# Kernel optimization log

Measured on AMD Instinct MI355X. Metric: run time of the kernel, lower is better.

The kernel has to match this reference:

```python
import jax, jax.numpy as jnp
import numpy as np

TEMPERATURE = 0.07
BASE_TEMPERATURE = 0.07


def _pairwise_euclid(x):
    # torch.cdist(x, x, p=2), with safe sqrt (zero grad at zero distance)
    sq = jnp.sum(x * x, axis=1)
    d2 = sq[:, None] + sq[None, :] - 2.0 * (x @ x.T)
    d2 = jnp.maximum(d2, 0.0)
    safe = jnp.where(d2 > 0.0, d2, 1.0)
    return jnp.where(d2 > 0.0, jnp.sqrt(safe), 0.0)


def setup_inputs() -> dict:
    key = jax.random.key(0)
    k1, k2 = jax.random.split(key)
    features = jax.random.normal(k1, (1024, 2, 512), dtype=jnp.float32)
    labels = jax.random.uniform(k2, (1024,), dtype=jnp.float32)
    return {"features": features, "labels": labels}


def reference(features, labels):
    B, V, D = features.shape
    N = B * V
    # torch.cat(torch.unbind(features, dim=1), dim=0): views stacked -> [N, D]
    cf = features.transpose(1, 0, 2).reshape(N, D)
    lab = jnp.tile(labels, V)  # label of row i is labels[i % B]

    dist = _pairwise_euclid(cf)              # [N, N]
    logits = -dist / TEMPERATURE
    eye = jnp.eye(N, dtype=logits.dtype)
    w = jnp.exp(logits) * (1.0 - eye)        # exp(logits) with l == i excluded

    dis = jnp.abs(lab[:, None] - lab[None, :])  # |y_i - y_j|, symmetric

    # negative[i, j] = sum_{l != i, |y_l - y_i| >= |y_i - y_j|} exp(logits[i, l])
    # computed per-row via sort + suffix cumsum + searchsorted (O(N^2 log N))
    order = jnp.argsort(dis, axis=1)
    sorted_d = jnp.take_along_axis(dis, order, axis=1)
    sorted_w = jnp.take_along_axis(w, order, axis=1)
    suffix = jnp.flip(jnp.cumsum(jnp.flip(sorted_w, axis=1), axis=1), axis=1)
    suffix = jnp.concatenate([suffix, jnp.zeros((N, 1), suffix.dtype)], axis=1)  # [N, N+1]
    # side='left': counts entries strictly < d, so suffix[idx] sums all >= d (ties incl.)
    idx = jax.vmap(lambda sd, d: jnp.searchsorted(sd, d, side='left'))(sorted_d, dis)
    negative = jnp.take_along_axis(suffix, idx, axis=1)
    negative = negative * (1.0 - eye) + eye  # diag set to 1 (log -> 0)

    logits_z = logits * (1.0 - eye)          # logits[i, i] = 0
    log_prob = logits_z - jnp.log(negative)
    mean_log_prob_pos = jnp.sum(log_prob, axis=1) / (N - 1)
    loss = -(TEMPERATURE / BASE_TEMPERATURE) * jnp.mean(mean_log_prob_pos)
    return loss
```

## Files before the change

kernel.cpp:

```cpp
#include <hip/hip_runtime.h>
#include <math.h>


#define NN 2048
#define BB 1024
#define DD 512
#define NT 256
#define NEGINF (-INFINITY)
#define CS 64.0f

typedef short s16x8 __attribute__((ext_vector_type(8)));
typedef float f32x4 __attribute__((ext_vector_type(4)));

__device__ __forceinline__ const float* cf_row(const float* F, int i) {
    return F + ((size_t)(i & (BB - 1)) * 2 + (size_t)(i >> 10)) * DD;
}

__device__ __forceinline__ unsigned bf_rne(float x) {
    const unsigned u = __float_as_uint(x);
    return (u + 0x7FFFu + ((u >> 16) & 1u)) >> 16;
}
__device__ __forceinline__ float bf_val(unsigned h) {
    return __uint_as_float(h << 16);
}

__global__ __launch_bounds__(256) void rank_sort_kernel(const float* __restrict__ labels,
                                                        float* __restrict__ slab,
                                                        int* __restrict__ sj) {
    __shared__ float lab[BB];
    const int t = threadIdx.x;
    #pragma unroll
    for (int e = 0; e < 4; ++e) lab[t + e * NT] = labels[t + e * NT];
    __syncthreads();
    const int p = blockIdx.x * NT + t;
    const float L = lab[p];
    int rank = 0;
    #pragma unroll 4
    for (int q4 = 0; q4 < BB / 4; ++q4) {
        const float4 l4 = reinterpret_cast<const float4*>(lab)[q4];
        const int q = q4 * 4;
        rank += (l4.x < L) || (l4.x == L && (q + 0) < p);
        rank += (l4.y < L) || (l4.y == L && (q + 1) < p);
        rank += (l4.z < L) || (l4.z == L && (q + 2) < p);
        rank += (l4.w < L) || (l4.w == L && (q + 3) < p);
    }
    slab[2 * rank] = L; slab[2 * rank + 1] = L;
    sj[2 * rank] = p;   sj[2 * rank + 1] = p + BB;
}

__global__ __launch_bounds__(256) void prep_split_kernel(const float* __restrict__ F,
                                                         ushort* __restrict__ Ahi,
                                                         ushort* __restrict__ Alo,
                                                         float* __restrict__ sq) {
    const int t = threadIdx.x;
    const int lane = t & 63;
    const int w = t >> 6;
    const int i = blockIdx.x * 4 + w;
    const float* src = cf_row(F, i);
    const float4 v0 = reinterpret_cast<const float4*>(src)[lane];
    const float4 v1 = reinterpret_cast<const float4*>(src)[lane + 64];
    float ss = v0.x * v0.x + v0.y * v0.y + v0.z * v0.z + v0.w * v0.w
             + v1.x * v1.x + v1.y * v1.y + v1.z * v1.z + v1.w * v1.w;
    #pragma unroll
    for (int st = 32; st > 0; st >>= 1) ss += __shfl_down(ss, st);
    if (lane == 0) sq[i] = ss;

    const float a[8] = {v0.x, v0.y, v0.z, v0.w, v1.x, v1.y, v1.z, v1.w};
    ushort h[8], l[8];
    #pragma unroll
    for (int e = 0; e < 8; ++e) {
        const unsigned hb = bf_rne(a[e]);
        h[e] = (ushort)hb;
        l[e] = (ushort)bf_rne(a[e] - bf_val(hb));
    }
    const size_t base = (size_t)i * DD;
    *reinterpret_cast<ushort4*>(&Ahi[base + lane * 4])       = make_ushort4(h[0], h[1], h[2], h[3]);
    *reinterpret_cast<ushort4*>(&Ahi[base + 256 + lane * 4]) = make_ushort4(h[4], h[5], h[6], h[7]);
    *reinterpret_cast<ushort4*>(&Alo[base + lane * 4])       = make_ushort4(l[0], l[1], l[2], l[3]);
    *reinterpret_cast<ushort4*>(&Alo[base + 256 + lane * 4]) = make_ushort4(l[4], l[5], l[6], l[7]);
}

#define GT 64
#define TK 32
__global__ __launch_bounds__(256) void gemm_dist_kernel(const ushort* __restrict__ Ahi,
                                                        const ushort* __restrict__ Alo,
                                                        const float* __restrict__ sq,
                                                        const int* __restrict__ sj,
                                                        float* __restrict__ distp) {
    __shared__ ushort Ah[4][GT][8];
    __shared__ ushort Al[4][GT][8];
    __shared__ ushort Bh[4][GT][8];
    __shared__ ushort Bl[4][GT][8];
    __shared__ int   sjcA[GT];
    __shared__ int   sjcB[GT];
    __shared__ float sqA[GT];
    __shared__ float sqB[GT];

    const int t = threadIdx.x;
    const int lane = t & 63;
    const int w = t >> 6;

    const int id = blockIdx.x;
    int by = (int)((__fsqrt_rn(8.0f * (float)id + 1.0f) - 1.0f) * 0.5f);
    while ((by + 1) * (by + 2) / 2 <= id) ++by;
    while (by * (by + 1) / 2 > id) --by;
    const int bx = id - by * (by + 1) / 2;
    const int row0 = by * GT;
    const int col0 = bx * GT;
    const bool diag = (bx == by);

    if (t < GT) {
        const int s = sj[row0 + t];
        sjcA[t] = s; sqA[t] = sq[s];
    } else if (t < 2 * GT) {
        const int u = t - GT;
        const int s = sj[col0 + u];
        sjcB[u] = s; sqB[u] = sq[s];
    }
    __syncthreads();
    const int rr = t >> 2;
    const int cq = t & 3;
    const size_t gA = (size_t)sjcA[rr] * DD + cq * 8;
    const size_t gB = (size_t)sjcB[rr] * DD + cq * 8;

    f32x4 acc[4] = {};
    const int m = lane & 15;
    const int q = lane >> 4;

    for (int kt = 0; kt < DD / TK; ++kt) {
        __syncthreads();
        const size_t ko = (size_t)kt * TK;
        *reinterpret_cast<int4*>(&Ah[cq][rr][0]) = *reinterpret_cast<const int4*>(&Ahi[gA + ko]);
        *reinterpret_cast<int4*>(&Al[cq][rr][0]) = *reinterpret_cast<const int4*>(&Alo[gA + ko]);
        *reinterpret_cast<int4*>(&Bh[cq][rr][0]) = *reinterpret_cast<const int4*>(&Ahi[gB + ko]);
        *reinterpret_cast<int4*>(&Bl[cq][rr][0]) = *reinterpret_cast<const int4*>(&Alo[gB + ko]);
        __syncthreads();

        const s16x8 fah = *reinterpret_cast<const s16x8*>(&Ah[q][w * 16 + m][0]);
        const s16x8 fal = *reinterpret_cast<const s16x8*>(&Al[q][w * 16 + m][0]);
        s16x8 fbh[4], fbl[4];
        #pragma unroll
        for (int nt = 0; nt < 4; ++nt) {
            fbh[nt] = *reinterpret_cast<const s16x8*>(&Bh[q][nt * 16 + m][0]);
            fbl[nt] = *reinterpret_cast<const s16x8*>(&Bl[q][nt * 16 + m][0]);
        }
        #pragma unroll
        for (int nt = 0; nt < 4; ++nt) {
            acc[nt] = __builtin_amdgcn_mfma_f32_16x16x32_bf16(fah, fbh[nt], acc[nt], 0, 0, 0);
            acc[nt] = __builtin_amdgcn_mfma_f32_16x16x32_bf16(fah, fbl[nt], acc[nt], 0, 0, 0);
            acc[nt] = __builtin_amdgcn_mfma_f32_16x16x32_bf16(fal, fbh[nt], acc[nt], 0, 0, 0);
        }
    }

    const int lr0 = w * 16 + q * 4;
    #pragma unroll
    for (int nt = 0; nt < 4; ++nt) {
        const int lc = nt * 16 + m;
        float o[4];
        #pragma unroll
        for (int r = 0; r < 4; ++r) {
            const float d2 = sqA[lr0 + r] + sqB[lc] - 2.0f * acc[nt][r];
            o[r] = (d2 > 0.f) ? sqrtf(d2) : 0.f;
        }
        #pragma unroll
        for (int r = 0; r < 4; ++r)
            distp[(size_t)(row0 + lr0 + r) * NN + col0 + lc] = o[r];
        if (!diag) {
            const float4 o4 = make_float4(o[0], o[1], o[2], o[3]);
            *reinterpret_cast<float4*>(&distp[(size_t)(col0 + lc) * NN + row0 + lr0]) = o4;
        }
    }
}

__device__ __forceinline__ int bs_right(const float* key, float d, int lo, int hi) {
    while (lo < hi) {
        const int mid = (lo + hi) >> 1;
        if (key[mid] >= d) hi = mid; else lo = mid + 1;
    }
    return lo;
}
__device__ __forceinline__ int bs_left(const float* key, float d, int lo, int hi) {
    while (lo < hi) {
        const int mid = (lo + hi) >> 1;
        if (key[mid] < d) hi = mid; else lo = mid + 1;
    }
    return lo;
}

__global__ __launch_bounds__(256) void row_kernel(const float* __restrict__ distp,
                                                  const float* __restrict__ slab,
                                                  double* __restrict__ rowval) {
    __shared__ float key[NN];
    __shared__ float Pf[NN];
    __shared__ float Sf[NN + 1];
    __shared__ float wmxA[4], wmxB[4], wps[4], wss[4];
    __shared__ double wDA[4], wLA[4], wDB[4], wLB[4];

    const int pr = blockIdx.x;
    const int rA = 2 * pr, rB = 2 * pr + 1;
    const int t = threadIdx.x;
    const int lane = t & 63;
    const int w = t >> 6;
    const float x = slab[rA];
    const float negInvT = -1.0f / 0.07f;
    const float* drowA = &distp[(size_t)rA * NN];
    const float* drowB = &distp[(size_t)rB * NN];

    #pragma unroll
    for (int e = 0; e < 2; ++e) {
        const int p4 = t + e * NT;
        const float4 l4 = reinterpret_cast<const float4*>(slab)[p4];
        key[p4 * 4 + 0] = fabsf(l4.x - x);
        key[p4 * 4 + 1] = fabsf(l4.y - x);
        key[p4 * 4 + 2] = fabsf(l4.z - x);
        key[p4 * 4 + 3] = fabsf(l4.w - x);
    }
    const int cb = t * 8;
    float vA[8], vB[8];
    double dsumA = 0.0, dsumB = 0.0;
    float mxA = NEGINF, mxB = NEGINF;
    #pragma unroll
    for (int e = 0; e < 2; ++e) {
        const float4 a4 = reinterpret_cast<const float4*>(drowA)[2 * t + e];
        const float4 b4 = reinterpret_cast<const float4*>(drowB)[2 * t + e];
        const float av[4] = {a4.x, a4.y, a4.z, a4.w};
        const float bv[4] = {b4.x, b4.y, b4.z, b4.w};
        #pragma unroll
        for (int c = 0; c < 4; ++c) {
            const int pc = cb + e * 4 + c;
            if (pc == rA) vA[e * 4 + c] = NEGINF;
            else { const float vv = av[c] * negInvT; vA[e * 4 + c] = vv; mxA = fmaxf(mxA, vv); dsumA += (double)av[c]; }
            if (pc == rB) vB[e * 4 + c] = NEGINF;
            else { const float vv = bv[c] * negInvT; vB[e * 4 + c] = vv; mxB = fmaxf(mxB, vv); dsumB += (double)bv[c]; }
        }
    }
    #pragma unroll
    for (int st = 32; st > 0; st >>= 1) {
        mxA = fmaxf(mxA, __shfl_down(mxA, st));
        mxB = fmaxf(mxB, __shfl_down(mxB, st));
    }
    if (lane == 0) { wmxA[w] = mxA; wmxB[w] = mxB; }
    __syncthreads();
    const float MA = fmaxf(fmaxf(wmxA[0], wmxA[1]), fmaxf(wmxA[2], wmxA[3]));
    const float MB = fmaxf(fmaxf(wmxB[0], wmxB[1]), fmaxf(wmxB[2], wmxB[3]));

    int L8[8], R8[8];
    const int a = cb, b = cb + 7;
    {
        const int le = (rA - 1 < b) ? rA - 1 : b;
        if (a <= le) {
            const float da = key[a];
            const int Ra = bs_right(key, da, rA, NN);
            int Rl = Ra;
            if (le > a) Rl = bs_right(key, key[le], rA, Ra);
            for (int p = a; p <= le; ++p) {
                const float d = key[p];
                int R;
                if (p == a) R = Ra;
                else if (p == le) R = Rl;
                else R = bs_right(key, d, Rl, Ra);
                int L = p + 1;
                while (L < rA && key[L] == d) ++L;
                L8[p - a] = L; R8[p - a] = R;
            }
        }
        const int rs = (rA + 1 > a) ? rA + 1 : a;
        if (rs <= b) {
            const float dr = key[rs];
            const int Lr = bs_left(key, dr, 0, rA);
            int Lb = Lr;
            if (b > rs) Lb = bs_left(key, key[b], 0, Lr);
            for (int p = rs; p <= b; ++p) {
                const float d = key[p];
                int L;
                if (p == rs) L = Lr;
                else if (p == b) L = Lb;
                else L = bs_left(key, d, Lb, Lr);
                int R = p;
                while (R > rA && key[R - 1] == d) --R;
                L8[p - a] = L; R8[p - a] = R;
            }
        }
        if (rA >= a && rA <= b) { L8[rA - a] = rA; R8[rA - a] = rA; }
    }

    double lnsumA = 0.0;
    {
        float e8[8];
        #pragma unroll
        for (int jj = 0; jj < 8; ++jj) e8[jj] = __expf(vA[jj] - MA + CS);
        {
            float run = 0.f, ex[8];
            #pragma unroll
            for (int jj = 0; jj < 8; ++jj) { ex[jj] = run; run += e8[jj]; }
            float inc = run;
            #pragma unroll
            for (int st = 1; st < 64; st <<= 1) {
                const float nm = __shfl_up(inc, st);
                if (lane >= st) inc += nm;
            }
            float xofs = __shfl_up(inc, 1);
            if (lane == 0) xofs = 0.f;
            if (lane == 63) wps[w] = inc;
            __syncthreads();
            #pragma unroll
            for (int ww = 0; ww < 3; ++ww)
                if (ww < w) xofs += wps[ww];
            #pragma unroll
            for (int jj = 0; jj < 8; ++jj) Pf[cb + jj] = ex[jj] + xofs;
        }
        {
            float run = 0.f, sx[8];
            #pragma unroll
            for (int jj = 7; jj >= 0; --jj) { run += e8[jj]; sx[jj] = run; }
            float inc = run;
            #pragma unroll
            for (int st = 1; st < 64; st <<= 1) {
                const float nm = __shfl_down(inc, st);
                if (lane + st < 64) inc += nm;
            }
            float xofs = __shfl_down(inc, 1);
            if (lane == 63) xofs = 0.f;
            if (lane == 0) wss[w] = inc;
            __syncthreads();
            #pragma unroll
            for (int ww = 1; ww < 4; ++ww)
                if (ww > w) xofs += wss[ww];
            #pragma unroll
            for (int jj = 0; jj < 8; ++jj) Sf[cb + jj] = sx[jj] + xofs;
            if (t == 0) Sf[NN] = 0.f;
        }
        __syncthreads();
        const float MBA = MA - CS;
        #pragma unroll
        for (int jj = 0; jj < 8; ++jj) {
            const int p = cb + jj;
            if (p == rA) continue;
            const float s = fmaxf(Pf[L8[jj]] + Sf[R8[jj]], 1e-38f);
            lnsumA += (double)(MBA + __logf(s));
        }
    }
    __syncthreads();

    double lnsumB = 0.0;
    {
        float e8[8];
        #pragma unroll
        for (int jj = 0; jj < 8; ++jj) e8[jj] = __expf(vB[jj] - MB + CS);
        {
            float run = 0.f, ex[8];
            #pragma unroll
            for (int jj = 0; jj < 8; ++jj) { ex[jj] = run; run += e8[jj]; }
            float inc = run;
            #pragma unroll
            for (int st = 1; st < 64; st <<= 1) {
                const float nm = __shfl_up(inc, st);
                if (lane >= st) inc += nm;
            }
            float xofs = __shfl_up(inc, 1);
            if (lane == 0) xofs = 0.f;
            if (lane == 63) wps[w] = inc;
            __syncthreads();
            #pragma unroll
            for (int ww = 0; ww < 3; ++ww)
                if (ww < w) xofs += wps[ww];
            #pragma unroll
            for (int jj = 0; jj < 8; ++jj) Pf[cb + jj] = ex[jj] + xofs;
        }
        {
            float run = 0.f, sx[8];
            #pragma unroll
            for (int jj = 7; jj >= 0; --jj) { run += e8[jj]; sx[jj] = run; }
            float inc = run;
            #pragma unroll
            for (int st = 1; st < 64; st <<= 1) {
                const float nm = __shfl_down(inc, st);
                if (lane + st < 64) inc += nm;
            }
            float xofs = __shfl_down(inc, 1);
            if (lane == 63) xofs = 0.f;
            if (lane == 0) wss[w] = inc;
            __syncthreads();
            #pragma unroll
            for (int ww = 1; ww < 4; ++ww)
                if (ww > w) xofs += wss[ww];
            #pragma unroll
            for (int jj = 0; jj < 8; ++jj) Sf[cb + jj] = sx[jj] + xofs;
            if (t == 0) Sf[NN] = 0.f;
        }
        __syncthreads();
        const float MBB = MB - CS;
        #pragma unroll
        for (int jj = 0; jj < 8; ++jj) {
            const int p = cb + jj;
            if (p == rB) continue;
            const float s = fmaxf(Pf[L8[jj]] + Sf[R8[jj]], 1e-38f);
            lnsumB += (double)(MBB + __logf(s));
        }
    }

    #pragma unroll
    for (int st = 32; st > 0; st >>= 1) {
        dsumA  += __shfl_down(dsumA, st);
        lnsumA += __shfl_down(lnsumA, st);
        dsumB  += __shfl_down(dsumB, st);
        lnsumB += __shfl_down(lnsumB, st);
    }
    if (lane == 0) { wDA[w] = dsumA; wLA[w] = lnsumA; wDB[w] = dsumB; wLB[w] = lnsumB; }
    __syncthreads();
    if (t == 0) {
        rowval[rA] = (-(wDA[0] + wDA[1] + wDA[2] + wDA[3]) / 0.07)
                   - (wLA[0] + wLA[1] + wLA[2] + wLA[3]);
        rowval[rB] = (-(wDB[0] + wDB[1] + wDB[2] + wDB[3]) / 0.07)
                   - (wLB[0] + wLB[1] + wLB[2] + wLB[3]);
    }
}

__global__ __launch_bounds__(256) void finalize_kernel(const double* __restrict__ rowval,
                                                       float* __restrict__ out) {
    __shared__ double red[NT];
    const int t = threadIdx.x;
    double s = 0.0;
    for (int j = t; j < NN; j += NT) s += rowval[j];
    red[t] = s;
    __syncthreads();
    for (int ofs = NT / 2; ofs > 0; ofs >>= 1) {
        if (t < ofs) red[t] += red[t + ofs];
        __syncthreads();
    }
    if (t == 0) {
        out[0] = (float)(-red[0] / ((double)NN * (double)(NN - 1)));
    }
}

extern "C" void kernel_launch(void* const* d_in, const int* in_sizes, int n_in,
                              void* d_out, int out_size, void* d_ws, size_t ws_size,
                              hipStream_t stream) {
    const float* features = (const float*)d_in[0];
    const float* labels   = (const float*)d_in[1];
    float* out = (float*)d_out;

    char* ws = (char*)d_ws;
    size_t off = 0;
    float*  sq     = (float*) (ws + off); off += NN * sizeof(float);
    float*  slab   = (float*) (ws + off); off += NN * sizeof(float);
    int*    sj     = (int*)   (ws + off); off += NN * sizeof(int);
    double* rowval = (double*)(ws + off); off += NN * sizeof(double);
    ushort* Ahi    = (ushort*)(ws + off); off += (size_t)NN * DD * sizeof(ushort);
    ushort* Alo    = (ushort*)(ws + off); off += (size_t)NN * DD * sizeof(ushort);
    float*  distp  = (float*) (ws + off); off += (size_t)NN * NN * sizeof(float);

    rank_sort_kernel<<<4, NT, 0, stream>>>(labels, slab, sj);
    prep_split_kernel<<<NN / 4, NT, 0, stream>>>(features, Ahi, Alo, sq);
    gemm_dist_kernel<<<32 * 33 / 2, NT, 0, stream>>>(Ahi, Alo, sq, sj, distp);
    row_kernel<<<NN / 2, NT, 0, stream>>>(distp, slab, rowval);
    finalize_kernel<<<1, NT, 0, stream>>>(rowval, out);
}
```

Before: 137.5 us.

## Fuse label-rank and prep kernels; double-buffer GEMM shared tiles

Merges the label ranking kernel and the bf16 hi/lo split kernel into one launch, using block index to select the role, removing a kernel launch. The distance GEMM now double-buffers its shared-memory K tiles with one barrier per iteration, loading the next tile while the MFMAs run on the current one. This doubles shared memory per block and adds register pressure for the in-flight loads.

After: 135.6 us. About the same (-1.4%).

```diff
diff --git a/kernel.cpp b/kernel.cpp
--- a/kernel.cpp
+++ b/kernel.cpp
@@ -6,6 +6,7 @@
 #define BB 1024
 #define DD 512
 #define NT 256
+#define NPREP 512
 #define NEGINF (-INFINITY)
 #define CS 64.0f
 
@@ -24,60 +25,60 @@
     return __uint_as_float(h << 16);
 }
 
-__global__ __launch_bounds__(256) void rank_sort_kernel(const float* __restrict__ labels,
-                                                        float* __restrict__ slab,
-                                                        int* __restrict__ sj) {
-    __shared__ float lab[BB];
+__global__ __launch_bounds__(256) void prep_kernel(const float* __restrict__ F,
+                                                   const float* __restrict__ labels,
+                                                   ushort* __restrict__ Ahi,
+                                                   ushort* __restrict__ Alo,
+                                                   float* __restrict__ sq,
+                                                   float* __restrict__ slab,
+                                                   int* __restrict__ sj) {
     const int t = threadIdx.x;
-    #pragma unroll
-    for (int e = 0; e < 4; ++e) lab[t + e * NT] = labels[t + e * NT];
-    __syncthreads();
-    const int p = blockIdx.x * NT + t;
-    const float L = lab[p];
-    int rank = 0;
-    #pragma unroll 4
-    for (int q4 = 0; q4 < BB / 4; ++q4) {
-        const float4 l4 = reinterpret_cast<const float4*>(lab)[q4];
-        const int q = q4 * 4;
-        rank += (l4.x < L) || (l4.x == L && (q + 0) < p);
-        rank += (l4.y < L) || (l4.y == L && (q + 1) < p);
-        rank += (l4.z < L) || (l4.z == L && (q + 2) < p);
-        rank += (l4.w < L) || (l4.w == L && (q + 3) < p);
-    }
-    slab[2 * rank] = L; slab[2 * rank + 1] = L;
-    sj[2 * rank] = p;   sj[2 * rank + 1] = p + BB;
-}
-
-__global__ __launch_bounds__(256) void prep_split_kernel(const float* __restrict__ F,
-                                                         ushort* __restrict__ Ahi,
-                                                         ushort* __restrict__ Alo,
-                                                         float* __restrict__ sq) {
-    const int t = threadIdx.x;
-    const int lane = t & 63;
-    const int w = t >> 6;
-    const int i = blockIdx.x * 4 + w;
-    const float* src = cf_row(F, i);
-    const float4 v0 = reinterpret_cast<const float4*>(src)[lane];
-    const float4 v1 = reinterpret_cast<const float4*>(src)[lane + 64];
-    float ss = v0.x * v0.x + v0.y * v0.y + v0.z * v0.z + v0.w * v0.w
-             + v1.x * v1.x + v1.y * v1.y + v1.z * v1.z + v1.w * v1.w;
-    #pragma unroll
-    for (int st = 32; st > 0; st >>= 1) ss += __shfl_down(ss, st);
-    if (lane == 0) sq[i] = ss;
-
-    const float a[8] = {v0.x, v0.y, v0.z, v0.w, v1.x, v1.y, v1.z, v1.w};
-    ushort h[8], l[8];
-    #pragma unroll
-    for (int e = 0; e < 8; ++e) {
-        const unsigned hb = bf_rne(a[e]);
-        h[e] = (ushort)hb;
-        l[e] = (ushort)bf_rne(a[e] - bf_val(hb));
-    }
-    const size_t base = (size_t)i * DD;
-    *reinterpret_cast<ushort4*>(&Ahi[base + lane * 4])       = make_ushort4(h[0], h[1], h[2], h[3]);
-    *reinterpret_cast<ushort4*>(&Ahi[base + 256 + lane * 4]) = make_ushort4(h[4], h[5], h[6], h[7]);
-    *reinterpret_cast<ushort4*>(&Alo[base + lane * 4])       = make_ushort4(l[0], l[1], l[2], l[3]);
-    *reinterpret_cast<ushort4*>(&Alo[base + 256 + lane * 4]) = make_ushort4(l[4], l[5], l[6], l[7]);
+    if (blockIdx.x < NPREP) {
+        const int lane = t & 63;
+        const int w = t >> 6;
+        const int i = blockIdx.x * 4 + w;
+        const float* src = cf_row(F, i);
+        const float4 v0 = reinterpret_cast<const float4*>(src)[lane];
+        const float4 v1 = reinterpret_cast<const float4*>(src)[lane + 64];
+        float ss = v0.x * v0.x + v0.y * v0.y + v0.z * v0.z + v0.w * v0.w
+                 + v1.x * v1.x + v1.y * v1.y + v1.z * v1.z + v1.w * v1.w;
+        #pragma unroll
+        for (int st = 32; st > 0; st >>= 1) ss += __shfl_down(ss, st);
+        if (lane == 0) sq[i] = ss;
+
+        const float a[8] = {v0.x, v0.y, v0.z, v0.w, v1.x, v1.y, v1.z, v1.w};
+        ushort h[8], l[8];
+        #pragma unroll
+        for (int e = 0; e < 8; ++e) {
+            const unsigned hb = bf_rne(a[e]);
+            h[e] = (ushort)hb;
+            l[e] = (ushort)bf_rne(a[e] - bf_val(hb));
+        }
+        const size_t base = (size_t)i * DD;
+        *reinterpret_cast<ushort4*>(&Ahi[base + lane * 4])       = make_ushort4(h[0], h[1], h[2], h[3]);
+        *reinterpret_cast<ushort4*>(&Ahi[base + 256 + lane * 4]) = make_ushort4(h[4], h[5], h[6], h[7]);
+        *reinterpret_cast<ushort4*>(&Alo[base + lane * 4])       = make_ushort4(l[0], l[1], l[2], l[3]);
+        *reinterpret_cast<ushort4*>(&Alo[base + 256 + lane * 4]) = make_ushort4(l[4], l[5], l[6], l[7]);
+    } else {
+        __shared__ float lab[BB];
+        #pragma unroll
+        for (int e = 0; e < 4; ++e) lab[t + e * NT] = labels[t + e * NT];
+        __syncthreads();
+        const int p = (blockIdx.x - NPREP) * NT + t;
+        const float L = lab[p];
+        int rank = 0;
+        #pragma unroll 4
+        for (int q4 = 0; q4 < BB / 4; ++q4) {
+            const float4 l4 = reinterpret_cast<const float4*>(lab)[q4];
+            const int q = q4 * 4;
+            rank += (l4.x < L) || (l4.x == L && (q + 0) < p);
+            rank += (l4.y < L) || (l4.y == L && (q + 1) < p);
+            rank += (l4.z < L) || (l4.z == L && (q + 2) < p);
+            rank += (l4.w < L) || (l4.w == L && (q + 3) < p);
+        }
+        slab[2 * rank] = L; slab[2 * rank + 1] = L;
+        sj[2 * rank] = p;   sj[2 * rank + 1] = p + BB;
+    }
 }
 
 #define GT 64
@@ -87,10 +88,10 @@
                                                         const float* __restrict__ sq,
                                                         const int* __restrict__ sj,
                                                         float* __restrict__ distp) {
-    __shared__ ushort Ah[4][GT][8];
-    __shared__ ushort Al[4][GT][8];
-    __shared__ ushort Bh[4][GT][8];
-    __shared__ ushort Bl[4][GT][8];
+    __shared__ ushort Ah[2][4][GT][8];
+    __shared__ ushort Al[2][4][GT][8];
+    __shared__ ushort Bh[2][4][GT][8];
+    __shared__ ushort Bl[2][4][GT][8];
     __shared__ int   sjcA[GT];
     __shared__ int   sjcB[GT];
     __shared__ float sqA[GT];
@@ -123,26 +124,36 @@
     const size_t gA = (size_t)sjcA[rr] * DD + cq * 8;
     const size_t gB = (size_t)sjcB[rr] * DD + cq * 8;
 
+    {
+        *reinterpret_cast<int4*>(&Ah[0][cq][rr][0]) = *reinterpret_cast<const int4*>(&Ahi[gA]);
+        *reinterpret_cast<int4*>(&Al[0][cq][rr][0]) = *reinterpret_cast<const int4*>(&Alo[gA]);
+        *reinterpret_cast<int4*>(&Bh[0][cq][rr][0]) = *reinterpret_cast<const int4*>(&Ahi[gB]);
+        *reinterpret_cast<int4*>(&Bl[0][cq][rr][0]) = *reinterpret_cast<const int4*>(&Alo[gB]);
+    }
+
     f32x4 acc[4] = {};
     const int m = lane & 15;
     const int q = lane >> 4;
-
-    for (int kt = 0; kt < DD / TK; ++kt) {
+    const int KT = DD / TK;
+
+    for (int kt = 0; kt < KT; ++kt) {
+        const int cur = kt & 1;
         __syncthreads();
-        const size_t ko = (size_t)kt * TK;
-        *reinterpret_cast<int4*>(&Ah[cq][rr][0]) = *reinterpret_cast<const int4*>(&Ahi[gA + ko]);
-        *reinterpret_cast<int4*>(&Al[cq][rr][0]) = *reinterpret_cast<const int4*>(&Alo[gA + ko]);
-        *reinterpret_cast<int4*>(&Bh[cq][rr][0]) = *reinterpret_cast<const int4*>(&Ahi[gB + ko]);
-        *reinterpret_cast<int4*>(&Bl[cq][rr][0]) = *reinterpret_cast<const int4*>(&Alo[gB + ko]);
-        __syncthreads();
-
-        const s16x8 fah = *reinterpret_cast<const s16x8*>(&Ah[q][w * 16 + m][0]);
-        const s16x8 fal = *reinterpret_cast<const s16x8*>(&Al[q][w * 16 + m][0]);
+        if (kt + 1 < KT) {
+            const size_t ko = (size_t)(kt + 1) * TK;
+            const int nxt = 1 - cur;
+            *reinterpret_cast<int4*>(&Ah[nxt][cq][rr][0]) = *reinterpret_cast<const int4*>(&Ahi[gA + ko]);
+            *reinterpret_cast<int4*>(&Al[nxt][cq][rr][0]) = *reinterpret_cast<const int4*>(&Alo[gA + ko]);
+            *reinterpret_cast<int4*>(&Bh[nxt][cq][rr][0]) = *reinterpret_cast<const int4*>(&Ahi[gB + ko]);
+            *reinterpret_cast<int4*>(&Bl[nxt][cq][rr][0]) = *reinterpret_cast<const int4*>(&Alo[gB + ko]);
+        }
+        const s16x8 fah = *reinterpret_cast<const s16x8*>(&Ah[cur][q][w * 16 + m][0]);
+        const s16x8 fal = *reinterpret_cast<const s16x8*>(&Al[cur][q][w * 16 + m][0]);
         s16x8 fbh[4], fbl[4];
         #pragma unroll
         for (int nt = 0; nt < 4; ++nt) {
-            fbh[nt] = *reinterpret_cast<const s16x8*>(&Bh[q][nt * 16 + m][0]);
-            fbl[nt] = *reinterpret_cast<const s16x8*>(&Bl[q][nt * 16 + m][0]);
+            fbh[nt] = *reinterpret_cast<const s16x8*>(&Bh[cur][q][nt * 16 + m][0]);
+            fbl[nt] = *reinterpret_cast<const s16x8*>(&Bl[cur][q][nt * 16 + m][0]);
         }
         #pragma unroll
         for (int nt = 0; nt < 4; ++nt) {
@@ -450,8 +461,7 @@
     ushort* Alo    = (ushort*)(ws + off); off += (size_t)NN * DD * sizeof(ushort);
     float*  distp  = (float*) (ws + off); off += (size_t)NN * NN * sizeof(float);
 
-    rank_sort_kernel<<<4, NT, 0, stream>>>(labels, slab, sj);
-    prep_split_kernel<<<NN / 4, NT, 0, stream>>>(features, Ahi, Alo, sq);
+    prep_kernel<<<NPREP + 4, NT, 0, stream>>>(features, labels, Ahi, Alo, sq, slab, sj);
     gemm_dist_kernel<<<32 * 33 / 2, NT, 0, stream>>>(Ahi, Alo, sq, sj, distp);
     row_kernel<<<NN / 2, NT, 0, stream>>>(distp, slab, rowval);
     finalize_kernel<<<1, NT, 0, stream>>>(rowval, out);
```
